# Kernel tuning notes

Hardware: AMD Instinct MI355X
Metric: run time of the kernel (lower is better)

Reference implementation:

```python
import jax, jax.numpy as jnp
import numpy as np

PIXEL_SIZE = 0.1
PI = 3.141592653589793


def setup_inputs() -> dict:
    key = jax.random.key(0)
    batch = jax.random.normal(key, (128, 1, 512, 512), dtype=jnp.float32)
    return {"batch": batch}


def _hann_window(roi):
    # lin = linspace(-roi/2, roi/2, roi); r[i,j] = sqrt(lin[j]^2 + lin[i]^2)
    lin = jnp.linspace(-roi / 2, roi / 2, roi, dtype=jnp.float32)
    r = jnp.sqrt(lin[None, :] ** 2 + lin[:, None] ** 2)
    hann = 0.5 * (1.0 + jnp.cos(PI * r / (roi / 2)))
    hann = jnp.where(r > roi / 2, 0.0, hann)
    return hann  # [roi, roi]


def _radial_segments(roi, n_freq):
    # radialDst = round(sqrt(xx^2 + yy^2)) with x = arange(-cx, roi-cx)
    cx = roi // 2
    x = np.arange(-cx, roi - cx, dtype=np.float64)
    xx, yy = np.meshgrid(x, x, indexing="ij")
    rad = np.round(np.sqrt(xx ** 2 + yy ** 2)).astype(np.int32)
    # bins >= n_freq go into an overflow segment that is discarded
    seg = np.where(rad < n_freq, rad, n_freq)
    return jnp.asarray(seg.ravel())


def reference(batch):
    px = PIXEL_SIZE
    roi = batch.shape[-1]
    cx = roi // 2
    n_freq = cx + 1
    nyquist = 1.0 / (2.0 * px)

    # subtract per-ROI mean
    batch_nm = batch - jnp.mean(batch, axis=(2, 3), keepdims=True)

    # Hann-windowed 2D power spectrum, averaged over realizations
    hann = _hann_window(roi)[None, None, :, :]
    F = jnp.fft.fftshift(jnp.fft.fft2(batch_nm * hann, axes=(2, 3)), axes=(2, 3))
    ps = jnp.mean(jnp.abs(F) ** 2, axis=0)            # [1, roi, roi]
    nps2D = (px ** 2 / roi ** 2) * jnp.squeeze(ps)    # [roi, roi]

    # single-pass radial mean binning (replaces per-k boolean-mask loop)
    seg = _radial_segments(roi, n_freq)
    flat = nps2D.ravel()
    sums = jax.ops.segment_sum(flat, seg, num_segments=n_freq + 1)[:n_freq]
    counts = jax.ops.segment_sum(jnp.ones_like(flat), seg, num_segments=n_freq + 1)[:n_freq]
    nps1D = sums / counts

    f1D = jnp.linspace(0.0, nyquist, n_freq, dtype=jnp.float32)
    return nps1D, nps2D, f1D
```

## Files before the change

kernel.cpp:

```cpp
#include <hip/hip_runtime.h>
#include <hip/hip_fp16.h>

#define N 512
#define NF 257
#define NB 128
#define PI_F 3.14159265358979323846f
#define C_SQ2 0.70710678118654752440f

__device__ __forceinline__ float2 cmul(float2 a, float2 b) {
    return make_float2(a.x * b.x - a.y * b.y, a.x * b.y + a.y * b.x);
}
__device__ __forceinline__ void bf(float2& a, float2& b) {
    float2 t = b;
    b = make_float2(a.x - t.x, a.y - t.y);
    a = make_float2(a.x + t.x, a.y + t.y);
}
__device__ __forceinline__ void bf_tw(float2& a, float2& b, float2 w) {
    float2 t = cmul(b, w);
    b = make_float2(a.x - t.x, a.y - t.y);
    a = make_float2(a.x + t.x, a.y + t.y);
}
__device__ __forceinline__ void bf_ni(float2& a, float2& b) {
    float2 t = make_float2(b.y, -b.x);
    b = make_float2(a.x - t.x, a.y - t.y);
    a = make_float2(a.x + t.x, a.y + t.y);
}
__device__ __forceinline__ void lds_order() {
    asm volatile("" ::: "memory");
}

__device__ __forceinline__ void fft_phaseA(float2 v[8]) {
    const float2 w64  = make_float2(C_SQ2, -C_SQ2);
    const float2 w192 = make_float2(-C_SQ2, -C_SQ2);
    bf(v[0], v[1]); bf(v[2], v[3]); bf(v[4], v[5]); bf(v[6], v[7]);
    bf(v[0], v[2]); bf_ni(v[1], v[3]); bf(v[4], v[6]); bf_ni(v[5], v[7]);
    bf(v[0], v[4]); bf_tw(v[1], v[5], w64); bf_ni(v[2], v[6]); bf_tw(v[3], v[7], w192);
}
__device__ __forceinline__ void fft_phaseBC(float2 v[8], float2 W1, float2 W1a,
                                            float2 W1n, float2 W1c, float2 W2,
                                            float2 W2n, float2 W3) {
    bf_tw(v[0], v[1], W3); bf_tw(v[2], v[3], W3); bf_tw(v[4], v[5], W3); bf_tw(v[6], v[7], W3);
    bf_tw(v[0], v[2], W2); bf_tw(v[1], v[3], W2n); bf_tw(v[4], v[6], W2); bf_tw(v[5], v[7], W2n);
    bf_tw(v[0], v[4], W1); bf_tw(v[1], v[5], W1a); bf_tw(v[2], v[6], W1n); bf_tw(v[3], v[7], W1c);
}

__device__ __forceinline__ void fft512_x2(float2 va[8], float2 vb[8], float2* st, int l) {
    const float2 w64  = make_float2(C_SQ2, -C_SQ2);
    const float2 w192 = make_float2(-C_SQ2, -C_SQ2);
    int g = l >> 3, r = l & 7;
    fft_phaseA(va); fft_phaseA(vb);
    lds_order();
#pragma unroll
    for (int e = 0; e < 8; e++) st[9 * l + e] = va[e];
    lds_order();
#pragma unroll
    for (int t = 0; t < 8; t++) va[t] = st[72 * g + 9 * t + r];
    lds_order();
#pragma unroll
    for (int e = 0; e < 8; e++) st[9 * l + e] = vb[e];
    lds_order();
#pragma unroll
    for (int t = 0; t < 8; t++) vb[t] = st[72 * g + 9 * t + r];
    float sn, cs;
    __sincosf(-(PI_F / 32.0f) * (float)r, &sn, &cs);
    float2 W1 = make_float2(cs, sn);
    float2 W2 = cmul(W1, W1);
    float2 W3 = cmul(W2, W2);
    float2 W2n = make_float2(W2.y, -W2.x);
    float2 W1a = cmul(W1, w64);
    float2 W1n = make_float2(W1.y, -W1.x);
    float2 W1c = cmul(W1, w192);
    fft_phaseBC(va, W1, W1a, W1n, W1c, W2, W2n, W3);
    fft_phaseBC(vb, W1, W1a, W1n, W1c, W2, W2n, W3);
    lds_order();
#pragma unroll
    for (int t = 0; t < 8; t++) st[72 * g + 9 * t + r] = va[t];
    lds_order();
#pragma unroll
    for (int t = 0; t < 8; t++) va[t] = st[72 * t + l + (l >> 3)];
    lds_order();
#pragma unroll
    for (int t = 0; t < 8; t++) st[72 * g + 9 * t + r] = vb[t];
    lds_order();
#pragma unroll
    for (int t = 0; t < 8; t++) vb[t] = st[72 * t + l + (l >> 3)];
    __sincosf(-(PI_F / 256.0f) * (float)l, &sn, &cs);
    float2 Wc = make_float2(cs, sn);
    float2 w2 = cmul(Wc, Wc);
    float2 w4 = cmul(w2, w2);
    float2 w2n = make_float2(w2.y, -w2.x);
    float2 Wca = cmul(Wc, w64);
    float2 Wcn = make_float2(Wc.y, -Wc.x);
    float2 Wcc = cmul(Wc, w192);
    fft_phaseBC(va, Wc, Wca, Wcn, Wcc, w2, w2n, w4);
    fft_phaseBC(vb, Wc, Wca, Wcn, Wcc, w2, w2n, w4);
}

__device__ __forceinline__ void unpack_rows(const float2 v[8], __half2* tile,
                                            int lr0, int lr1, int l, int sl) {
#pragma unroll
    for (int t = 0; t <= 4; t++) {
        float2 a = v[7 - t];
        float zfx = __shfl(a.x, sl);
        float zfy = __shfl(a.y, sl);
        if (l == 0) { float2 o = v[(8 - t) & 7]; zfx = o.x; zfy = o.y; }
        float2 z = v[t];
        int col = 64 * t + l;
        if (col < NF) {
            tile[lr0 * 265 + col] = __floats2half2_rn(0.5f * (z.x + zfx), 0.5f * (z.y - zfy));
            tile[lr1 * 265 + col] = __floats2half2_rn(0.5f * (z.y + zfy), 0.5f * (zfx - z.x));
        }
    }
}

__device__ __forceinline__ void unpack_rows_store(const float2 v[8], float2* __restrict__ Hrow,
                                                  int r0, int r1, int l, int sl) {
#pragma unroll
    for (int t = 0; t <= 4; t++) {
        float2 a = v[7 - t];
        float zfx = __shfl(a.x, sl);
        float zfy = __shfl(a.y, sl);
        if (l == 0) { float2 o = v[(8 - t) & 7]; zfx = o.x; zfy = o.y; }
        float2 z = v[t];
        int col = 64 * t + l;
        if (col < NF) {
            Hrow[(size_t)col * N + r0] = make_float2(0.5f * (z.x + zfx), 0.5f * (z.y - zfy));
            Hrow[(size_t)col * N + r1] = make_float2(0.5f * (z.y + zfy), 0.5f * (zfx - z.x));
        }
    }
}

__global__ __launch_bounds__(256) void hanntab_zero_kernel(float* __restrict__ htab,
                                                           float* __restrict__ accH,
                                                           float* __restrict__ bins,
                                                           float* __restrict__ meanacc) {
    int i = blockIdx.x * 256 + threadIdx.x;
    int r = i >> 9, c = i & (N - 1);
    const float step = (float)N / (float)(N - 1);
    float a = -0.5f * (float)N + (float)r * step;
    float b = -0.5f * (float)N + (float)c * step;
    float rr = sqrtf(a * a + b * b);
    float h = (rr > 256.0f) ? 0.0f : 0.5f * (1.0f + cosf(rr * (PI_F / 256.0f)));
    htab[i] = h;
    if (i < NF * N) accH[i] = 0.0f;
    if (i < 2 * (NF + 1)) bins[i] = 0.0f;
    if (i < NB) meanacc[i] = 0.0f;
}

__global__ __launch_bounds__(256, 8) void rowfft_kernel(const float* __restrict__ x,
                                                        const float* __restrict__ htab,
                                                        float* __restrict__ meanacc,
                                                        __half2* __restrict__ inter,
                                                        float2* __restrict__ Hrow) {
    __shared__ __align__(16) float sm[4608];
    __shared__ float redsum[4];
    int tid = threadIdx.x;
    int w = tid >> 6, l = tid & 63;
    int rl = __brev((unsigned)l) >> 26;
    const int bre[8] = {0, 4, 2, 6, 1, 5, 3, 7};
    float2* st = (float2*)sm + w * 576;
    int sl = (64 - l) & 63;

    if (blockIdx.x >= NB * 32) {
        int hb = blockIdx.x - NB * 32;
        int r1 = (hb << 4) + 4 * w;
        const float* hp = htab + (size_t)r1 * N + rl;
        float hx[4][8];
#pragma unroll
        for (int j = 0; j < 4; j++)
#pragma unroll
            for (int e = 0; e < 8; e++) hx[j][e] = hp[j * N + (bre[e] << 6)];
        float2 va[8], vb[8];
#pragma unroll
        for (int e = 0; e < 8; e++) {
            va[e] = make_float2(hx[0][e], hx[1][e]);
            vb[e] = make_float2(hx[2][e], hx[3][e]);
        }
        fft512_x2(va, vb, st, l);
        unpack_rows_store(va, Hrow, r1, r1 + 1, l, sl);
        unpack_rows_store(vb, Hrow, r1 + 2, r1 + 3, l, sl);
        return;
    }

    int img = blockIdx.x >> 5;
    int rowbase = (blockIdx.x & 31) << 4;
    int r1 = rowbase + 4 * w;
    const float* xp = x + ((size_t)img * N + r1) * N + rl;
    const float* hp = htab + (size_t)r1 * N + rl;

    float ax[4][8], hx[4][8];
#pragma unroll
    for (int j = 0; j < 4; j++)
#pragma unroll
        for (int e = 0; e < 8; e++) ax[j][e] = xp[j * N + (bre[e] << 6)];
#pragma unroll
    for (int j = 0; j < 4; j++)
#pragma unroll
        for (int e = 0; e < 8; e++) hx[j][e] = hp[j * N + (bre[e] << 6)];

    float rsum = 0.0f;
#pragma unroll
    for (int j = 0; j < 4; j++)
#pragma unroll
        for (int e = 0; e < 8; e++) rsum += ax[j][e];

    float2 va[8], vb[8];
#pragma unroll
    for (int e = 0; e < 8; e++) {
        va[e] = make_float2(ax[0][e] * hx[0][e], ax[1][e] * hx[1][e]);
        vb[e] = make_float2(ax[2][e] * hx[2][e], ax[3][e] * hx[3][e]);
    }

#pragma unroll
    for (int off = 32; off > 0; off >>= 1) rsum += __shfl_down(rsum, off);
    if (l == 0) redsum[w] = rsum;

    fft512_x2(va, vb, st, l);
    __syncthreads();
    if (tid == 0) {
        float s = 0.0f;
#pragma unroll
        for (int i = 0; i < 4; i++) s += redsum[i];
        atomicAdd(meanacc + img, s);
    }

    __half2* tile = (__half2*)sm;
    unpack_rows(va, tile, 4 * w, 4 * w + 1, l, sl);
    unpack_rows(vb, tile, 4 * w + 2, 4 * w + 3, l, sl);
    __syncthreads();

    int c0 = tid >> 4, rr = tid & 15;
#pragma unroll
    for (int it = 0; it < 17; it++) {
        int c = it * 16 + c0;
        if (c < NF) {
            inter[((size_t)img * NF + c) * N + rowbase + rr] = tile[rr * 265 + c];
        }
    }
}

__global__ __launch_bounds__(256, 4) void colfft_kernel(const __half2* __restrict__ inter,
                                                        const float2* __restrict__ Hrow,
                                                        const float* __restrict__ meanacc,
                                                        float* __restrict__ accH) {
    __shared__ __align__(16) float sm[4608];
    int tid = threadIdx.x;
    int w = tid >> 6, l = tid & 63;
    int col = blockIdx.x * 4 + w;
    int colc = col < NF ? col : NF - 1;
    int b0 = blockIdx.y * 4;
    float2* st = (float2*)sm + w * 576;
    int rl = __brev((unsigned)l) >> 26;
    const int bre[8] = {0, 4, 2, 6, 1, 5, 3, 7};

    float2 hc[8];
    const float2* hp = Hrow + (size_t)colc * N + rl;
#pragma unroll
    for (int e = 0; e < 8; e++) hc[e] = hp[bre[e] << 6];

    float mn[4];
#pragma unroll
    for (int i = 0; i < 4; i++)
        mn[i] = meanacc[b0 + i] * (1.0f / ((float)N * (float)N));

    float pw[8];
#pragma unroll
    for (int t = 0; t < 8; t++) pw[t] = 0.0f;

    const size_t istr = (size_t)NF * N;
    const __half2* base = inter + ((size_t)b0 * NF + colc) * N + rl;

    __half2 cA[8], cB[8], nA[8], nB[8];
#pragma unroll
    for (int e = 0; e < 8; e++) {
        cA[e] = base[bre[e] << 6];
        cB[e] = base[istr + (bre[e] << 6)];
    }
    __builtin_amdgcn_sched_barrier(0);

#pragma unroll
    for (int it = 0; it < 2; it++) {
        if (it == 0) {
#pragma unroll
            for (int e = 0; e < 8; e++) {
                nA[e] = base[2 * istr + (bre[e] << 6)];
                nB[e] = base[3 * istr + (bre[e] << 6)];
            }
        }
        float mA = mn[2 * it], mB = mn[2 * it + 1];
        float2 va[8], vb[8];
#pragma unroll
        for (int e = 0; e < 8; e++) {
            float2 zA = __half22float2(cA[e]);
            float2 zB = __half22float2(cB[e]);
            va[e] = make_float2(zA.x - mA * hc[e].x, zA.y - mA * hc[e].y);
            vb[e] = make_float2(zB.x - mB * hc[e].x, zB.y - mB * hc[e].y);
        }
        fft512_x2(va, vb, st, l);
#pragma unroll
        for (int t = 0; t < 8; t++)
            pw[t] += va[t].x * va[t].x + va[t].y * va[t].y
                   + vb[t].x * vb[t].x + vb[t].y * vb[t].y;
#pragma unroll
        for (int e = 0; e < 8; e++) { cA[e] = nA[e]; cB[e] = nB[e]; }
    }

    if (col < NF) {
#pragma unroll
        for (int t = 0; t < 8; t++)
            atomicAdd(&accH[(size_t)col * N + 64 * t + l], pw[t]);
    }
}

__global__ __launch_bounds__(256) void finalize2d_kernel(const float* __restrict__ accH,
                                                         float* __restrict__ out2d,
                                                         float* __restrict__ bins) {
    __shared__ float lsum[NF];
    __shared__ float lcnt[NF];
    int t = threadIdx.x;
    for (int i = t; i < NF; i += 256) { lsum[i] = 0.0f; lcnt[i] = 0.0f; }
    __syncthreads();
    const float scale = (0.1f * 0.1f) / ((float)N * (float)N) / (float)NB;
    int idx = blockIdx.x * 256 + t;
    int stride = gridDim.x * 256;
    for (int p = idx; p < N * N; p += stride) {
        int i = p >> 9, j = p & (N - 1);
        int jm = (j + 256) & 511;
        int col, k;
        if (jm < NF) { col = jm; k = (i + 256) & 511; }
        else         { col = 256 - j; k = (256 - i) & 511; }
        float v = accH[((size_t)col << 9) + k] * scale;
        out2d[p] = v;
        float xi = (float)(i - 256), yj = (float)(j - 256);
        int rad = (int)rintf(sqrtf(xi * xi + yj * yj));
        if (rad < NF) { atomicAdd(&lsum[rad], v); atomicAdd(&lcnt[rad], 1.0f); }
    }
    __syncthreads();
    for (int i = t; i < NF; i += 256) {
        if (lsum[i] != 0.0f || lcnt[i] != 0.0f) {
            atomicAdd(&bins[i], lsum[i]);
            atomicAdd(&bins[NF + 1 + i], lcnt[i]);
        }
    }
}

__global__ void finalize1d_kernel(const float* __restrict__ bins, float* __restrict__ out) {
    int t = blockIdx.x * blockDim.x + threadIdx.x;
    if (t < NF) {
        out[t] = bins[t] / bins[NF + 1 + t];
        out[NF + N * N + t] = (float)t * (5.0f / 256.0f);
    }
}

extern "C" void kernel_launch(void* const* d_in, const int* in_sizes, int n_in,
                              void* d_out, int out_size, void* d_ws, size_t ws_size,
                              hipStream_t stream) {
    const float* x = (const float*)d_in[0];
    float* out = (float*)d_out;
    char* ws = (char*)d_ws;

    float* accH    = (float*)ws;
    float* meanacc = (float*)(ws + (size_t)NF * N * sizeof(float));
    float* bins    = meanacc + NB;
    size_t off_h = (size_t)NF * N * sizeof(float) + NB * sizeof(float)
                   + 2 * (NF + 1) * sizeof(float);
    off_h = (off_h + 255) & ~(size_t)255;
    float2* Hrow = (float2*)(ws + off_h);
    size_t off_t = off_h + (size_t)NF * N * sizeof(float2);
    off_t = (off_t + 255) & ~(size_t)255;
    float* htab = (float*)(ws + off_t);
    size_t off_inter = off_t + (size_t)N * N * sizeof(float);
    off_inter = (off_inter + 255) & ~(size_t)255;
    __half2* inter = (__half2*)(ws + off_inter);

    hanntab_zero_kernel<<<dim3(N * N / 256), dim3(256), 0, stream>>>(htab, accH, bins, meanacc);
    rowfft_kernel<<<dim3(NB * 32 + 32), dim3(256), 0, stream>>>(x, htab, meanacc, inter, Hrow);
    colfft_kernel<<<dim3(65, 32), dim3(256), 0, stream>>>(inter, Hrow, meanacc, accH);
    finalize2d_kernel<<<dim3(512), dim3(256), 0, stream>>>(accH, out + NF, bins);
    finalize1d_kernel<<<dim3(2), dim3(256), 0, stream>>>(bins, out);
}
```

Measured before the change: 295.9 us.

## Compute Hann window inline in row FFT and double rows per block

Removes the precomputed Hann table, so the row-FFT kernel computes window values directly with sqrtf and the fast __cosf instead of loading them from global memory. The row-FFT block size goes from 256 to 512 threads, covering 32 rows per block, which halves the grid and the number of mean atomics. The zero kernel no longer writes a table. The trade is extra ALU and transcendental work per element in place of table loads, a larger shared-memory footprint per block, and slightly lower accuracy from __cosf.

```diff
diff --git a/kernel.cpp b/kernel.cpp
--- a/kernel.cpp
+++ b/kernel.cpp
@@ -130,46 +130,49 @@
     }
 }
 
-__global__ __launch_bounds__(256) void hanntab_zero_kernel(float* __restrict__ htab,
-                                                           float* __restrict__ accH,
-                                                           float* __restrict__ bins,
-                                                           float* __restrict__ meanacc) {
-    int i = blockIdx.x * 256 + threadIdx.x;
-    int r = i >> 9, c = i & (N - 1);
-    const float step = (float)N / (float)(N - 1);
-    float a = -0.5f * (float)N + (float)r * step;
-    float b = -0.5f * (float)N + (float)c * step;
-    float rr = sqrtf(a * a + b * b);
-    float h = (rr > 256.0f) ? 0.0f : 0.5f * (1.0f + cosf(rr * (PI_F / 256.0f)));
-    htab[i] = h;
+__global__ void zero_kernel(float* __restrict__ accH, float* __restrict__ bins,
+                            float* __restrict__ meanacc) {
+    int i = blockIdx.x * blockDim.x + threadIdx.x;
     if (i < NF * N) accH[i] = 0.0f;
     if (i < 2 * (NF + 1)) bins[i] = 0.0f;
     if (i < NB) meanacc[i] = 0.0f;
 }
 
-__global__ __launch_bounds__(256, 8) void rowfft_kernel(const float* __restrict__ x,
-                                                        const float* __restrict__ htab,
+__global__ __launch_bounds__(512, 6) void rowfft_kernel(const float* __restrict__ x,
                                                         float* __restrict__ meanacc,
                                                         __half2* __restrict__ inter,
                                                         float2* __restrict__ Hrow) {
-    __shared__ __align__(16) float sm[4608];
-    __shared__ float redsum[4];
+    __shared__ __align__(16) float sm[9216];
+    __shared__ float redsum[8];
     int tid = threadIdx.x;
     int w = tid >> 6, l = tid & 63;
     int rl = __brev((unsigned)l) >> 26;
     const int bre[8] = {0, 4, 2, 6, 1, 5, 3, 7};
     float2* st = (float2*)sm + w * 576;
     int sl = (64 - l) & 63;
-
-    if (blockIdx.x >= NB * 32) {
-        int hb = blockIdx.x - NB * 32;
-        int r1 = (hb << 4) + 4 * w;
-        const float* hp = htab + (size_t)r1 * N + rl;
+    const float step = (float)N / (float)(N - 1);
+
+    float bb[8];
+#pragma unroll
+    for (int e = 0; e < 8; e++) {
+        float b = (float)((bre[e] << 6) + rl) * step - 256.0f;
+        bb[e] = b * b;
+    }
+
+    if (blockIdx.x >= NB * 16) {
+        int hb = blockIdx.x - NB * 16;
+        int r1 = (hb << 5) + 4 * w;
         float hx[4][8];
 #pragma unroll
-        for (int j = 0; j < 4; j++)
-#pragma unroll
-            for (int e = 0; e < 8; e++) hx[j][e] = hp[j * N + (bre[e] << 6)];
+        for (int j = 0; j < 4; j++) {
+            float a = (float)(r1 + j) * step - 256.0f;
+            float aa = a * a;
+#pragma unroll
+            for (int e = 0; e < 8; e++) {
+                float rr = sqrtf(aa + bb[e]);
+                hx[j][e] = (rr > 256.0f) ? 0.0f : 0.5f * (1.0f + __cosf(rr * (PI_F / 256.0f)));
+            }
+        }
         float2 va[8], vb[8];
 #pragma unroll
         for (int e = 0; e < 8; e++) {
@@ -182,21 +185,28 @@
         return;
     }
 
-    int img = blockIdx.x >> 5;
-    int rowbase = (blockIdx.x & 31) << 4;
+    int img = blockIdx.x >> 4;
+    int rowbase = (blockIdx.x & 15) << 5;
     int r1 = rowbase + 4 * w;
     const float* xp = x + ((size_t)img * N + r1) * N + rl;
-    const float* hp = htab + (size_t)r1 * N + rl;
-
-    float ax[4][8], hx[4][8];
+
+    float ax[4][8];
 #pragma unroll
     for (int j = 0; j < 4; j++)
 #pragma unroll
         for (int e = 0; e < 8; e++) ax[j][e] = xp[j * N + (bre[e] << 6)];
-#pragma unroll
-    for (int j = 0; j < 4; j++)
-#pragma unroll
-        for (int e = 0; e < 8; e++) hx[j][e] = hp[j * N + (bre[e] << 6)];
+
+    float hx[4][8];
+#pragma unroll
+    for (int j = 0; j < 4; j++) {
+        float a = (float)(r1 + j) * step - 256.0f;
+        float aa = a * a;
+#pragma unroll
+        for (int e = 0; e < 8; e++) {
+            float rr = sqrtf(aa + bb[e]);
+            hx[j][e] = (rr > 256.0f) ? 0.0f : 0.5f * (1.0f + __cosf(rr * (PI_F / 256.0f)));
+        }
+    }
 
     float rsum = 0.0f;
 #pragma unroll
@@ -220,7 +230,7 @@
     if (tid == 0) {
         float s = 0.0f;
 #pragma unroll
-        for (int i = 0; i < 4; i++) s += redsum[i];
+        for (int i = 0; i < 8; i++) s += redsum[i];
         atomicAdd(meanacc + img, s);
     }
 
@@ -229,7 +239,7 @@
     unpack_rows(vb, tile, 4 * w + 2, 4 * w + 3, l, sl);
     __syncthreads();
 
-    int c0 = tid >> 4, rr = tid & 15;
+    int c0 = tid >> 5, rr = tid & 31;
 #pragma unroll
     for (int it = 0; it < 17; it++) {
         int c = it * 16 + c0;
@@ -366,15 +376,12 @@
                    + 2 * (NF + 1) * sizeof(float);
     off_h = (off_h + 255) & ~(size_t)255;
     float2* Hrow = (float2*)(ws + off_h);
-    size_t off_t = off_h + (size_t)NF * N * sizeof(float2);
-    off_t = (off_t + 255) & ~(size_t)255;
-    float* htab = (float*)(ws + off_t);
-    size_t off_inter = off_t + (size_t)N * N * sizeof(float);
+    size_t off_inter = off_h + (size_t)NF * N * sizeof(float2);
     off_inter = (off_inter + 255) & ~(size_t)255;
     __half2* inter = (__half2*)(ws + off_inter);
 
-    hanntab_zero_kernel<<<dim3(N * N / 256), dim3(256), 0, stream>>>(htab, accH, bins, meanacc);
-    rowfft_kernel<<<dim3(NB * 32 + 32), dim3(256), 0, stream>>>(x, htab, meanacc, inter, Hrow);
+    zero_kernel<<<dim3((NF * N + 255) / 256), dim3(256), 0, stream>>>(accH, bins, meanacc);
+    rowfft_kernel<<<dim3(NB * 16 + 16), dim3(512), 0, stream>>>(x, meanacc, inter, Hrow);
     colfft_kernel<<<dim3(65, 32), dim3(256), 0, stream>>>(inter, Hrow, meanacc, accH);
     finalize2d_kernel<<<dim3(512), dim3(256), 0, stream>>>(accH, out + NF, bins);
     finalize1d_kernel<<<dim3(2), dim3(256), 0, stream>>>(bins, out);
```

Measured after the change: 253.8 us (median of 2 runs). -14.2%, faster.
